# Optimization experiments

Measured on AMD Instinct MI355X. Metric: run time of the kernel, lower is better.

The kernel has to match this reference:

```python
import jax, jax.numpy as jnp
import numpy as np

EMBED_DIM = 1024
NUM_HEADS = 16
HEAD_DIM = EMBED_DIM // NUM_HEADS  # 64, == n_wires of quantum kernel


def setup_inputs() -> dict:
    key = jax.random.key(0)
    k1, k2, k3, k4 = jax.random.split(key, 4)
    B, S = 2, 2048
    x = jax.random.normal(k1, (B, S, EMBED_DIM), dtype=jnp.float32)
    # fused QKV projection (no bias); PyTorch Linear stores [out, in]
    qkv_w = jax.random.normal(k2, (3 * EMBED_DIM, EMBED_DIM), dtype=jnp.float32) / np.sqrt(EMBED_DIM)
    out_w = jax.random.normal(k3, (EMBED_DIM, EMBED_DIM), dtype=jnp.float32) / np.sqrt(EMBED_DIM)
    # one trainable RY angle per wire (shared across q, k, v and all heads)
    qparams = jax.random.normal(k4, (HEAD_DIM,), dtype=jnp.float32)
    return {"x": x, "qkv_w": qkv_w, "out_w": out_w, "qparams": qparams}


def _split_heads(t):
    B, S, E = t.shape
    return t.reshape(B, S, NUM_HEADS, HEAD_DIM).transpose(0, 2, 1, 3)  # [B,H,S,D]


def _apply_quantum(t, qparams):
    # RX(x_i)|0> then RY(p_i), measure <Z> on each wire independently:
    # <Z> = cos(x_i) * cos(p_i) -- separable single-qubit circuit reduces to trig.
    return jnp.cos(t) * jnp.cos(qparams)  # broadcast over last dim D


def reference(x, qkv_w, out_w, qparams):
    B, S, E = x.shape
    proj = x @ qkv_w.T                       # [B,S,3E]
    q, k, v = jnp.split(proj, 3, axis=-1)    # each [B,S,E]
    q = _apply_quantum(_split_heads(q), qparams)  # [B,H,S,D]
    k = _apply_quantum(_split_heads(k), qparams)
    v = _apply_quantum(_split_heads(v), qparams)
    scores = jnp.einsum('bhqd,bhkd->bhqk', q, k) / np.sqrt(HEAD_DIM)
    attn = jax.nn.softmax(scores, axis=-1)   # dropout is identity in eval
    out = jnp.einsum('bhqk,bhkd->bhqd', attn, v)  # [B,H,S,D]
    out = out.transpose(0, 2, 1, 3).reshape(B, S, E)
    return out @ out_w.T
```

## Files before the change

kernel.cpp:

```cpp
#include <hip/hip_runtime.h>
#include <hip/hip_bf16.h>

#define S_LEN 2048
#define EMB 1024
#define NH 16
#define HD 64

typedef __attribute__((ext_vector_type(8))) __bf16 bf16x8;
typedef __attribute__((ext_vector_type(4))) float f32x4;
typedef __attribute__((ext_vector_type(16))) float f32x16;
typedef __attribute__((ext_vector_type(4))) unsigned int u32x4;

__device__ inline void gload_lds16(const void* g, void* l) {
    __builtin_amdgcn_global_load_lds(
        (const __attribute__((address_space(1))) unsigned int*)g,
        (__attribute__((address_space(3))) unsigned int*)l, 16, 0, 0);
}

__global__ __launch_bounds__(256) void cvt_all(
    const float* __restrict__ x, const float* __restrict__ wq,
    const float* __restrict__ wo,
    __hip_bfloat16* __restrict__ xb, __hip_bfloat16* __restrict__ wqb,
    __hip_bfloat16* __restrict__ wob)
{
    const long C_X = (long)4096 * 1024 / 4;
    const long C_WQ = (long)3072 * 1024 / 4;
    long c = (long)blockIdx.x * 256 + threadIdx.x;
    const float* in;
    __hip_bfloat16* out;
    if (c < C_X) { in = x; out = xb; }
    else if (c < C_X + C_WQ) { in = wq; out = wqb; c -= C_X; }
    else { in = wo; out = wob; c -= C_X + C_WQ; }
    long i = c * 4;
    float4 v = *(const float4*)(in + i);
    __hip_bfloat16 b0 = __float2bfloat16(v.x);
    __hip_bfloat16 b1 = __float2bfloat16(v.y);
    __hip_bfloat16 b2 = __float2bfloat16(v.z);
    __hip_bfloat16 b3 = __float2bfloat16(v.w);
    ushort4 o = {*(unsigned short*)&b0, *(unsigned short*)&b1,
                 *(unsigned short*)&b2, *(unsigned short*)&b3};
    *(ushort4*)(out + i) = o;
}

template <int EPI, int BN, int NX, int CH>
__global__ __launch_bounds__(256) void gemm_mfma(
    const __hip_bfloat16* __restrict__ A,
    const __hip_bfloat16* __restrict__ B,
    const float* __restrict__ qp,
    __hip_bfloat16* __restrict__ Q,
    __hip_bfloat16* __restrict__ Kp,
    __hip_bfloat16* __restrict__ Vt,
    float* __restrict__ C)
{
    const int Kd = 1024;
    const int NI = BN / 32;
    __shared__ __align__(16) char Ash[128 * 128];
    __shared__ __align__(16) char Bsh[BN * 128];

    const int bid = blockIdx.x;
    const int sw_ = (bid & 7) * CH + (bid >> 3);
    const int m0 = (sw_ / NX) * 128;
    const int n0 = (sw_ % NX) * BN;

    const int t  = threadIdx.x;
    const int w  = t >> 6;
    const int l  = t & 63;
    const int lg = l >> 4, lm = l & 15;
    const int wr = w >> 1, wc = w & 1;

    const int r8 = l >> 3;
    const int sb = ((l & 7) * 16) ^ (r8 << 4);
    const char* srcA = (const char*)A + ((long)(m0 + w * 32 + r8) * Kd) * 2 + sb;
    const char* srcB = (const char*)B + ((long)(n0 + w * (BN / 4) + r8) * Kd) * 2 + sb;

    f32x4 acc[4][NI];
#pragma unroll
    for (int i = 0; i < 4; i++)
#pragma unroll
        for (int j = 0; j < NI; j++) acc[i][j] = (f32x4){0.f, 0.f, 0.f, 0.f};

    for (int kt = 0; kt < Kd * 2; kt += 128) {
#pragma unroll
        for (int j = 0; j < 4; j++)
            gload_lds16(srcA + (long)j * 8 * Kd * 2 + kt, Ash + (w * 32 + j * 8) * 128);
#pragma unroll
        for (int j = 0; j < NI; j++)
            gload_lds16(srcB + (long)j * 8 * Kd * 2 + kt,
                        Bsh + (w * (BN / 4) + j * 8) * 128);
        __syncthreads();
#pragma unroll
        for (int kk = 0; kk < 2; kk++) {
            bf16x8 af[4], bfr[NI];
            const int sw = (lm & 7) << 4;
            const int co = (kk * 64 + lg * 16);
#pragma unroll
            for (int mi = 0; mi < 4; mi++)
                af[mi] = *(const bf16x8*)(Ash + (wr * 64 + mi * 16 + lm) * 128 + (co ^ sw));
#pragma unroll
            for (int ni = 0; ni < NI; ni++)
                bfr[ni] = *(const bf16x8*)(Bsh + (wc * (BN / 2) + ni * 16 + lm) * 128 + (co ^ sw));
#pragma unroll
            for (int mi = 0; mi < 4; mi++)
#pragma unroll
                for (int ni = 0; ni < NI; ni++)
                    acc[mi][ni] = __builtin_amdgcn_mfma_f32_16x16x32_bf16(
                        af[mi], bfr[ni], acc[mi][ni], 0, 0, 0);
        }
        __syncthreads();
    }

    if constexpr (EPI == 0) {
        const int which = n0 >> 10;
        float cqp[NI];
#pragma unroll
        for (int ni = 0; ni < NI; ni++)
            cqp[ni] = __cosf(qp[(wc * (BN / 2) + ni * 16 + lm) & 63]);

        if (which == 2) {
            char* T = (w < 2 ? Ash : Bsh) + (w & 1) * 8192;
#pragma unroll
            for (int mi = 0; mi < 4; mi++)
#pragma unroll
                for (int r = 0; r < 4; r++)
#pragma unroll
                    for (int ni = 0; ni < NI; ni++) {
                        int row = ni * 16 + lm;
                        int col = mi * 16 + lg * 4 + r;
                        float val = __cosf(acc[mi][ni][r]) * cqp[ni];
                        *(__hip_bfloat16*)(T + row * 128 +
                                           ((col * 2) ^ ((row & 7) << 4))) =
                            __float2bfloat16(val);
                    }
            const int h  = ((n0 & 1023) >> 6) + wc;
            const int bh = (m0 >> 11) * NH + h;
            const int sbase = (m0 & 2047) + wr * 64;
#pragma unroll
            for (int j = 0; j < 8; j++) {
                int c = j * 64 + l;
                int d = c >> 3;
                int sc = (c & 7) * 16;
                uint4 v = *(const uint4*)(T + d * 128 + (sc ^ ((d & 7) << 4)));
                *(uint4*)((char*)(Vt + ((long)bh * HD + d) * S_LEN + sbase) + sc) = v;
            }
        } else {
#pragma unroll
            for (int mi = 0; mi < 4; mi++) {
#pragma unroll
                for (int r = 0; r < 4; r++) {
                    int m = m0 + wr * 64 + mi * 16 + lg * 4 + r;
                    int b = m >> 11, s = m & 2047;
#pragma unroll
                    for (int ni = 0; ni < NI; ni++) {
                        int n = n0 + wc * (BN / 2) + ni * 16 + lm;
                        int d = n & 63;
                        int h = (n & 1023) >> 6;
                        int bh = b * NH + h;
                        float val = __cosf(acc[mi][ni][r]) * cqp[ni];
                        if (which == 0)
                            Q[((long)bh * S_LEN + s) * HD + d] =
                                __float2bfloat16(val * 0.180336880f);
                        else
                            Kp[((long)bh * S_LEN + s) * HD + d] = __float2bfloat16(val);
                    }
                }
            }
        }
    } else {
#pragma unroll
        for (int mi = 0; mi < 4; mi++)
#pragma unroll
            for (int r = 0; r < 4; r++) {
                int m = m0 + wr * 64 + mi * 16 + lg * 4 + r;
#pragma unroll
                for (int ni = 0; ni < NI; ni++) {
                    int n = n0 + wc * (BN / 2) + ni * 16 + lm;
                    C[(long)m * 1024 + n] = acc[mi][ni][r];
                }
            }
    }
}

__global__ __launch_bounds__(256, 4) void attn_mfma(
    const __hip_bfloat16* __restrict__ Q,
    const __hip_bfloat16* __restrict__ K,
    const __hip_bfloat16* __restrict__ Vt,
    __hip_bfloat16* __restrict__ O)
{
    __shared__ __align__(16) char Ksh[2][64 * 128];
    __shared__ __align__(16) char Vsh[2][64 * 128];

    const int L  = blockIdx.x;
    const int bh = (L & 7) + (L >> 8) * 8;
    const int q0 = ((L >> 3) & 31) * 64;
    const int b  = bh >> 4, h = bh & 15;
    const int t  = threadIdx.x;
    const int w  = t >> 6;
    const int qi = w & 1;
    const int ki = w >> 1;
    const int l  = t & 63;
    const int lo5 = l & 31;
    const int hi  = l >> 5;

    const char* Qr =
        (const char*)(Q + ((long)bh * S_LEN + q0 + qi * 32 + lo5) * HD);
    bf16x8 qf[4];
#pragma unroll
    for (int ks = 0; ks < 4; ks++)
        qf[ks] = *(const bf16x8*)(Qr + ks * 32 + hi * 16);

    f32x16 oacc[2] = {};
    float lsum = 0.f;
    const float EXPB = 11.54156033f;

    const char* Kgb = (const char*)(K + (long)bh * S_LEN * HD);
    const char* Vgb = (const char*)(Vt + (long)bh * HD * S_LEN);

    const int swb = ((l & 7) * 16) ^ (((l >> 3) & 7) << 4);
    const int row0 = w * 8 + (l >> 3);
    const char* Ksrc  = Kgb + (long)row0 * 128 + swb;
    const char* Vsrc0 = Vgb + (long)row0 * (S_LEN * 2) + swb;
    const char* Vsrc1 = Vgb + (long)(row0 + 32) * (S_LEN * 2) + swb;

    gload_lds16(Ksrc, Ksh[0] + w * 1024);
    gload_lds16(Ksrc + 32 * 128, Ksh[0] + w * 1024 + 4096);
    gload_lds16(Vsrc0, Vsh[0] + w * 1024);
    gload_lds16(Vsrc1, Vsh[0] + w * 1024 + 4096);

    const int swr = (lo5 & 7) << 4;
    int cur = 0;
    for (int kt = 0; kt < S_LEN; kt += 64) {
        __syncthreads();

        if (kt + 64 < S_LEN) {
            int nk = kt + 64;
            gload_lds16(Ksrc + (long)nk * 128, Ksh[cur ^ 1] + w * 1024);
            gload_lds16(Ksrc + (long)(nk + 32) * 128, Ksh[cur ^ 1] + w * 1024 + 4096);
            gload_lds16(Vsrc0 + (long)nk * 2, Vsh[cur ^ 1] + w * 1024);
            gload_lds16(Vsrc1 + (long)nk * 2, Vsh[cur ^ 1] + w * 1024 + 4096);
        }

        const char* Kc = Ksh[cur];
        const char* Vc = Vsh[cur];

        f32x16 s;
#pragma unroll
        for (int r = 0; r < 16; r++) s[r] = -EXPB;
        const char* Krow = Kc + (ki * 32 + lo5) * 128;
        __builtin_amdgcn_s_setprio(1);
#pragma unroll
        for (int ks = 0; ks < 4; ks++) {
            bf16x8 kf = *(const bf16x8*)(Krow + ((ks * 32 + hi * 16) ^ swr));
            s = __builtin_amdgcn_mfma_f32_32x32x16_bf16(kf, qf[ks], s, 0, 0, 0);
        }
        __builtin_amdgcn_s_setprio(0);

        float p[16];
#pragma unroll
        for (int r = 0; r < 16; r++) p[r] = __builtin_amdgcn_exp2f(s[r]);
#pragma unroll
        for (int r = 0; r < 16; r += 4)
            lsum += (p[r] + p[r + 1]) + (p[r + 2] + p[r + 3]);
        unsigned c0, c1, c2, c3, c4, c5, c6, c7;
        asm("v_cvt_pk_bf16_f32 %0, %1, %2" : "=v"(c0) : "v"(p[0]),  "v"(p[1]));
        asm("v_cvt_pk_bf16_f32 %0, %1, %2" : "=v"(c1) : "v"(p[2]),  "v"(p[3]));
        asm("v_cvt_pk_bf16_f32 %0, %1, %2" : "=v"(c2) : "v"(p[4]),  "v"(p[5]));
        asm("v_cvt_pk_bf16_f32 %0, %1, %2" : "=v"(c3) : "v"(p[6]),  "v"(p[7]));
        asm("v_cvt_pk_bf16_f32 %0, %1, %2" : "=v"(c4) : "v"(p[8]),  "v"(p[9]));
        asm("v_cvt_pk_bf16_f32 %0, %1, %2" : "=v"(c5) : "v"(p[10]), "v"(p[11]));
        asm("v_cvt_pk_bf16_f32 %0, %1, %2" : "=v"(c6) : "v"(p[12]), "v"(p[13]));
        asm("v_cvt_pk_bf16_f32 %0, %1, %2" : "=v"(c7) : "v"(p[14]), "v"(p[15]));
        asm("v_permlane32_swap_b32 %0, %1" : "+v"(c0), "+v"(c2));
        asm("v_permlane32_swap_b32 %0, %1" : "+v"(c1), "+v"(c3));
        asm("v_permlane32_swap_b32 %0, %1" : "+v"(c4), "+v"(c6));
        asm("v_permlane32_swap_b32 %0, %1" : "+v"(c5), "+v"(c7));
        u32x4 w0 = {c0, c1, c2, c3};
        u32x4 w1 = {c4, c5, c6, c7};
        bf16x8 pa0 = __builtin_bit_cast(bf16x8, w0);
        bf16x8 pa1 = __builtin_bit_cast(bf16x8, w1);

        __builtin_amdgcn_s_setprio(1);
#pragma unroll
        for (int db = 0; db < 2; db++) {
            const char* Vrow = Vc + (db * 32 + lo5) * 128;
            bf16x8 vf0 = *(const bf16x8*)(Vrow + ((ki * 64 + hi * 16) ^ swr));
            bf16x8 vf1 = *(const bf16x8*)(Vrow + ((ki * 64 + 32 + hi * 16) ^ swr));
            oacc[db] = __builtin_amdgcn_mfma_f32_32x32x16_bf16(pa0, vf0, oacc[db], 0, 0, 0);
            oacc[db] = __builtin_amdgcn_mfma_f32_32x32x16_bf16(pa1, vf1, oacc[db], 0, 0, 0);
        }
        __builtin_amdgcn_s_setprio(0);
        cur ^= 1;
    }

    lsum += __shfl_xor(lsum, 32, 64);
    __syncthreads();
    float* Osh = (float*)Ksh;
    float* Lsh = (float*)Vsh;
    if (ki == 1) {
        float* dst = Osh + qi * 2048;
#pragma unroll
        for (int db = 0; db < 2; db++)
#pragma unroll
            for (int r = 0; r < 16; r++)
                dst[(db * 16 + r) * 64 + l] = oacc[db][r];
        Lsh[qi * 64 + l] = lsum;
    }
    __syncthreads();
    if (ki == 0) {
        const float* src = Osh + qi * 2048;
#pragma unroll
        for (int db = 0; db < 2; db++)
#pragma unroll
            for (int r = 0; r < 16; r++)
                oacc[db][r] += src[(db * 16 + r) * 64 + l];
        lsum += Lsh[qi * 64 + l];
        float inv = 1.f / lsum;
#pragma unroll
        for (int r = 0; r < 16; r++) {
            int qr = (r & 3) + 8 * (r >> 2) + 4 * hi;
            float invr = __shfl(inv, qr, 32);
            int qrow = q0 + qi * 32 + qr;
            long base = ((long)b * S_LEN + qrow) * EMB + h * HD;
            O[base + lo5]      = __float2bfloat16(oacc[0][r] * invr);
            O[base + 32 + lo5] = __float2bfloat16(oacc[1][r] * invr);
        }
    }
}

extern "C" void kernel_launch(void* const* d_in, const int* in_sizes, int n_in,
                              void* d_out, int out_size, void* d_ws, size_t ws_size,
                              hipStream_t stream) {
    const float* x     = (const float*)d_in[0];
    const float* qkv_w = (const float*)d_in[1];
    const float* out_w = (const float*)d_in[2];
    const float* qp    = (const float*)d_in[3];
    float* out = (float*)d_out;

    const long NELEM = (long)2 * S_LEN * EMB;
    __hip_bfloat16* Q   = (__hip_bfloat16*)d_ws;
    __hip_bfloat16* K   = Q + NELEM;
    __hip_bfloat16* Vt  = K + NELEM;
    __hip_bfloat16* O   = Vt + NELEM;
    __hip_bfloat16* xb  = O + NELEM;
    __hip_bfloat16* wqb = xb + NELEM;
    __hip_bfloat16* wob = wqb + (long)3072 * 1024;

    dim3 blk(256);
    cvt_all<<<dim3(8192), blk, 0, stream>>>(x, qkv_w, out_w, xb, wqb, wob);
    gemm_mfma<0, 128, 24, 96><<<dim3(768), blk, 0, stream>>>(
        xb, wqb, qp, Q, K, Vt, nullptr);
    attn_mfma<<<dim3(1024), blk, 0, stream>>>(Q, K, Vt, O);
    gemm_mfma<1, 64, 16, 64><<<dim3(512), blk, 0, stream>>>(
        O, wob, nullptr, nullptr, nullptr, nullptr, out);
}
```

Before: 115.7 us.

## Triple-buffer K/V tiles and software-pipeline QK^T one tile ahead of softmax/PV

Replaces the double-buffered K/V LDS staging with a three-stage ring buffer that prefetches two tiles ahead. The QK^T MFMA for the next tile is issued before the exp/convert/PV work of the current tile, so matrix and transcendental work can interleave and load latency is better hidden. It also moves the barrier to the end of each iteration. In exchange LDS use rises to 48KB per block and launch bounds drop to 3 blocks per CU, which lowers occupancy and adds register pressure from the extra score accumulator.

```diff
diff --git a/kernel.cpp b/kernel.cpp
--- a/kernel.cpp
+++ b/kernel.cpp
@@ -180,14 +180,13 @@
     }
 }
 
-__global__ __launch_bounds__(256, 4) void attn_mfma(
+__global__ __launch_bounds__(256, 3) void attn_mfma(
     const __hip_bfloat16* __restrict__ Q,
     const __hip_bfloat16* __restrict__ K,
     const __hip_bfloat16* __restrict__ Vt,
     __hip_bfloat16* __restrict__ O)
 {
-    __shared__ __align__(16) char Ksh[2][64 * 128];
-    __shared__ __align__(16) char Vsh[2][64 * 128];
+    __shared__ __align__(16) char smem[3 * 16384];
 
     const int L  = blockIdx.x;
     const int bh = (L & 7) + (L >> 8) * 8;
@@ -221,27 +220,18 @@
     const char* Vsrc0 = Vgb + (long)row0 * (S_LEN * 2) + swb;
     const char* Vsrc1 = Vgb + (long)(row0 + 32) * (S_LEN * 2) + swb;
 
-    gload_lds16(Ksrc, Ksh[0] + w * 1024);
-    gload_lds16(Ksrc + 32 * 128, Ksh[0] + w * 1024 + 4096);
-    gload_lds16(Vsrc0, Vsh[0] + w * 1024);
-    gload_lds16(Vsrc1, Vsh[0] + w * 1024 + 4096);
+#define STAGE(buf, nk)                                                         \
+    do {                                                                       \
+        char* base_ = smem + (buf) * 16384;                                    \
+        gload_lds16(Ksrc + (long)(nk) * 128, base_ + w * 1024);                \
+        gload_lds16(Ksrc + (long)((nk) + 32) * 128, base_ + w * 1024 + 4096);  \
+        gload_lds16(Vsrc0 + (long)(nk) * 2, base_ + 8192 + w * 1024);          \
+        gload_lds16(Vsrc1 + (long)(nk) * 2, base_ + 8192 + w * 1024 + 4096);   \
+    } while (0)
 
     const int swr = (lo5 & 7) << 4;
-    int cur = 0;
-    for (int kt = 0; kt < S_LEN; kt += 64) {
-        __syncthreads();
-
-        if (kt + 64 < S_LEN) {
-            int nk = kt + 64;
-            gload_lds16(Ksrc + (long)nk * 128, Ksh[cur ^ 1] + w * 1024);
-            gload_lds16(Ksrc + (long)(nk + 32) * 128, Ksh[cur ^ 1] + w * 1024 + 4096);
-            gload_lds16(Vsrc0 + (long)nk * 2, Vsh[cur ^ 1] + w * 1024);
-            gload_lds16(Vsrc1 + (long)nk * 2, Vsh[cur ^ 1] + w * 1024 + 4096);
-        }
-
-        const char* Kc = Ksh[cur];
-        const char* Vc = Vsh[cur];
-
+
+    auto QK = [&](const char* Kc) {
         f32x16 s;
 #pragma unroll
         for (int r = 0; r < 16; r++) s[r] = -EXPB;
@@ -253,10 +243,25 @@
             s = __builtin_amdgcn_mfma_f32_32x32x16_bf16(kf, qf[ks], s, 0, 0, 0);
         }
         __builtin_amdgcn_s_setprio(0);
+        return s;
+    };
+
+    STAGE(0, 0);
+    STAGE(1, 64);
+    __syncthreads();
+    f32x16 sp = QK(smem);
+
+    int cur = 0, nxt = 1, stg = 2;
+    for (int kt = 0; kt < S_LEN; kt += 64) {
+        const bool more = (kt + 64 < S_LEN);
+        if (kt + 128 < S_LEN) STAGE(stg, kt + 128);
+
+        f32x16 sn;
+        if (more) sn = QK(smem + nxt * 16384);
 
         float p[16];
 #pragma unroll
-        for (int r = 0; r < 16; r++) p[r] = __builtin_amdgcn_exp2f(s[r]);
+        for (int r = 0; r < 16; r++) p[r] = __builtin_amdgcn_exp2f(sp[r]);
 #pragma unroll
         for (int r = 0; r < 16; r += 4)
             lsum += (p[r] + p[r + 1]) + (p[r + 2] + p[r + 3]);
@@ -278,6 +283,7 @@
         bf16x8 pa0 = __builtin_bit_cast(bf16x8, w0);
         bf16x8 pa1 = __builtin_bit_cast(bf16x8, w1);
 
+        const char* Vc = smem + cur * 16384 + 8192;
         __builtin_amdgcn_s_setprio(1);
 #pragma unroll
         for (int db = 0; db < 2; db++) {
@@ -288,13 +294,17 @@
             oacc[db] = __builtin_amdgcn_mfma_f32_32x32x16_bf16(pa1, vf1, oacc[db], 0, 0, 0);
         }
         __builtin_amdgcn_s_setprio(0);
-        cur ^= 1;
-    }
+
+        __syncthreads();
+        int tmp = cur; cur = nxt; nxt = stg; stg = tmp;
+        if (more) sp = sn;
+    }
+#undef STAGE
 
     lsum += __shfl_xor(lsum, 32, 64);
     __syncthreads();
-    float* Osh = (float*)Ksh;
-    float* Lsh = (float*)Vsh;
+    float* Osh = (float*)smem;
+    float* Lsh = (float*)(smem + 16384);
     if (ki == 1) {
         float* dst = Osh + qi * 2048;
 #pragma unroll
```

New measurement: 120.6 us. 1.04x slower.
